# Performance work log

Hardware: AMD Instinct MI355X
Metric: run time of the kernel (lower is better)

Reference implementation:

```python
import jax, jax.numpy as jnp
import numpy as np

N = 8192
D = 2048      # input_dim
DH = 1024     # input_dim // r
DO = 1024     # output_dim

def setup_inputs() -> dict:
    key = jax.random.key(0)
    ks = jax.random.split(key, 11)
    s_in = 1.0 / np.sqrt(D)
    s_h = 1.0 / np.sqrt(DH)
    return {
        "O0": jax.random.normal(ks[0], (N, D), dtype=jnp.float32),
        "Ww": jax.random.uniform(ks[1], (DH, D), jnp.float32, -s_in, s_in),
        "Wb": jax.random.uniform(ks[2], (DH,), jnp.float32, -s_in, s_in),
        "Uw": jax.random.uniform(ks[3], (DH, D), jnp.float32, -s_in, s_in),
        "Ub": jax.random.uniform(ks[4], (DH,), jnp.float32, -s_in, s_in),
        "Hw": jax.random.uniform(ks[5], (DH, D), jnp.float32, -s_in, s_in),
        "Hb": jax.random.uniform(ks[6], (DH,), jnp.float32, -s_in, s_in),
        "fc0w": jax.random.uniform(ks[7], (D, DH), jnp.float32, -s_h, s_h),
        "fc0b": jax.random.uniform(ks[8], (D,), jnp.float32, -s_h, s_h),
        "fc1w": jax.random.uniform(ks[9], (DO, D), jnp.float32, -s_in, s_in),
        "fc1b": jax.random.uniform(ks[10], (DO,), jnp.float32, -s_in, s_in),
    }

def reference(O0, Ww, Wb, Uw, Ub, Hw, Hb, fc0w, fc0b, fc1w, fc1b):
    q = O0 @ Ww.T + Wb              # [N, DH]
    k = O0 @ Uw.T + Ub              # [N, DH]
    v = O0 @ Hw.T + Hb              # [N, DH]
    scores = q @ k.T                # [N, N], unscaled as in the original
    R1 = jax.nn.softmax(scores, axis=1)
    ctx = R1 @ v                    # [N, DH]
    O1 = O0 + (ctx @ fc0w.T + fc0b) # residual, [N, D]
    O2 = O1 @ fc1w.T + fc1b         # [N, DO]
    return (O1, O2)
```

## Files before the change

### kernel.cpp

```cpp
#include <hip/hip_runtime.h>
#include <cstdint>
#include <cstddef>

typedef _Float16 f16;
typedef _Float16 f16x8 __attribute__((ext_vector_type(8)));
typedef _Float16 f16x4 __attribute__((ext_vector_type(4)));
typedef float    f32x4 __attribute__((ext_vector_type(4)));

template <int V> struct IC { static constexpr int v = V; };

__global__ __launch_bounds__(256) void cvt_f32_f16(const float* __restrict__ in,
                                                   f16* __restrict__ out, int n) {
  int i = (blockIdx.x * 256 + threadIdx.x) * 4;
  if (i < n) {
    float4 v = *(const float4*)(in + i);
    f16x4 h; h[0] = (f16)v.x; h[1] = (f16)v.y; h[2] = (f16)v.z; h[3] = (f16)v.w;
    *(f16x4*)(out + i) = h;
  }
}

__global__ __launch_bounds__(256) void transpose_f16(const f16* __restrict__ in,
                                                     int ldi,
                                                     f16* __restrict__ out,
                                                     int R, int C) {
  __shared__ f16 tile[64][65];
  const int r0 = blockIdx.y * 64, c0 = blockIdx.x * 64;
  const int t = threadIdx.x;
#pragma unroll
  for (int p = 0; p < 2; p++) {
    int s = t + p * 256;
    int r = s >> 3, q = s & 7;
    f16x8 v = *(const f16x8*)(in + (size_t)(r0 + r) * ldi + c0 + q * 8);
#pragma unroll
    for (int e = 0; e < 8; e++) tile[r][q * 8 + e] = v[e];
  }
  __syncthreads();
#pragma unroll
  for (int p = 0; p < 2; p++) {
    int s = t + p * 256;
    int r = s >> 3, q = s & 7;
    f16x8 v;
#pragma unroll
    for (int e = 0; e < 8; e++) v[e] = tile[q * 8 + e][r];
    *(f16x8*)(out + (size_t)(c0 + r) * R + r0 + q * 8) = v;
  }
}

template <int MODE>
__global__ __launch_bounds__(512, 2) void gemm256(
    const f16* __restrict__ A, const f16* __restrict__ B,
    int M, int N, int K, int lda, int ldb,
    const float* __restrict__ bias,
    f16* __restrict__ outH, int ldo,
    float* __restrict__ statsM, float* __restrict__ statsS, int sld,
    const float* __restrict__ alphaT,
    const float* __restrict__ resid, int ldr,
    float* __restrict__ outF, int ldof) {
  __shared__ f16 lA[2][2][128 * 64];
  __shared__ f16 lB[2][2][128 * 64];
  __shared__ float lAl[2][256];

  const int t = threadIdx.x;
  const int wave = t >> 6, lane = t & 63;
  const int wr = wave >> 2, wc = wave & 3;
  const int quad = lane >> 4, l16 = lane & 15;
  const int rc = lane >> 3;
  const int kcs = (lane & 7) ^ rc;

  const int nwg = gridDim.x * gridDim.y;
  const int bid = blockIdx.y * gridDim.x + blockIdx.x;
  const int sb = (bid & 7) * (nwg >> 3) + (bid >> 3);
  const int bx = sb % gridDim.x, by = sb / gridDim.x;
  const int m0 = by * 256, n0 = bx * 256;
  const int nk = K >> 6;

  const f16* Abase = A + (size_t)m0 * lda;
  const f16* Bbase = B + (size_t)n0 * ldb;

  auto stageA = [&](int tau, int h) {
    if (tau >= nk) return;
    const f16* src = Abase + (size_t)(h * 128 + rc) * lda + tau * 64 + kcs * 8;
    f16* dstu = &lA[tau & 1][h][0];
#pragma unroll
    for (int j = 0; j < 2; j++) {
      const int sl = j * 8 + wave;
      __builtin_amdgcn_global_load_lds(
          (const __attribute__((address_space(1))) void*)(src + (size_t)sl * 8 * lda),
          (__attribute__((address_space(3))) void*)(dstu + sl * 512), 16, 0, 0);
    }
  };
  auto stageB = [&](int tau, int h) {
    if (tau >= nk) return;
    const f16* src = Bbase + (size_t)(h * 128 + rc) * ldb + tau * 64 + kcs * 8;
    f16* dstu = &lB[tau & 1][h][0];
#pragma unroll
    for (int j = 0; j < 2; j++) {
      const int sl = j * 8 + wave;
      __builtin_amdgcn_global_load_lds(
          (const __attribute__((address_space(1))) void*)(src + (size_t)sl * 8 * ldb),
          (__attribute__((address_space(3))) void*)(dstu + sl * 512), 16, 0, 0);
    }
  };
  auto stageAl = [&](int tau) {
    if constexpr (MODE == 2) {
      if (tau >= nk) return;
      __builtin_amdgcn_global_load_lds(
          (const __attribute__((address_space(1))) void*)(alphaT + (size_t)tau * M + m0 + lane * 4),
          (__attribute__((address_space(3))) void*)(&lAl[tau & 1][0]), 16, 0, 0);
    }
  };

  f32x4 acc[2][4][2][2];
#pragma unroll
  for (int mh = 0; mh < 2; mh++)
#pragma unroll
    for (int i = 0; i < 4; i++)
#pragma unroll
      for (int nh = 0; nh < 2; nh++)
#pragma unroll
        for (int j = 0; j < 2; j++)
#pragma unroll
          for (int e = 0; e < 4; e++) acc[mh][i][nh][j][e] = 0.0f;

  f16x8 af[4][2];
  f16x8 bf[2][2][2];

  auto readA = [&](auto BUFC, auto MHC) {
    constexpr int buf = decltype(BUFC)::v;
    constexpr int mh = decltype(MHC)::v;
#pragma unroll
    for (int i = 0; i < 4; i++) {
      const int r = i * 32 + wr * 16 + l16;
#pragma unroll
      for (int s = 0; s < 2; s++) {
        const int p = ((s * 4 + quad) ^ (l16 & 7)) * 8;
        af[i][s] = *(const f16x8*)(&lA[buf][mh][r * 64 + p]);
      }
      if constexpr (MODE == 2) {
        const f16 ah = (f16)lAl[buf][mh * 128 + r];
        af[i][0] = af[i][0] * ah;
        af[i][1] = af[i][1] * ah;
      }
    }
  };
  auto readB = [&](auto BUFC, auto NHC) {
    constexpr int buf = decltype(BUFC)::v;
    constexpr int nh = decltype(NHC)::v;
    const int hb = wc >> 1;
#pragma unroll
    for (int j = 0; j < 2; j++) {
      const int r = (wc & 1) * 64 + nh * 32 + j * 16 + l16;
#pragma unroll
      for (int s = 0; s < 2; s++) {
        const int p = ((s * 4 + quad) ^ (l16 & 7)) * 8;
        bf[nh][j][s] = *(const f16x8*)(&lB[buf][hb][r * 64 + p]);
      }
    }
  };
  auto mfmaQ = [&](auto MHC, auto NHC) {
    constexpr int mh = decltype(MHC)::v;
    constexpr int nh = decltype(NHC)::v;
    __builtin_amdgcn_s_setprio(1);
#pragma unroll
    for (int i = 0; i < 4; i++)
#pragma unroll
      for (int j = 0; j < 2; j++)
#pragma unroll
        for (int s = 0; s < 2; s++)
          acc[mh][i][nh][j] = __builtin_amdgcn_mfma_f32_16x16x32_f16(
              af[i][s], bf[nh][j][s], acc[mh][i][nh][j], 0, 0, 0);
    __builtin_amdgcn_s_setprio(0);
  };

  auto tile4 = [&](auto BUFC, int tt, bool dr) {
    readA(BUFC, IC<0>{});
    readB(BUFC, IC<0>{});
    stageA(tt + 1, 1);
    stageAl(tt + 1);
    __builtin_amdgcn_s_barrier();
    asm volatile("s_waitcnt lgkmcnt(0)" ::: "memory");
    mfmaQ(IC<0>{}, IC<0>{});
    __builtin_amdgcn_s_barrier();
    readB(BUFC, IC<1>{});
    stageA(tt + 2, 0);
    __builtin_amdgcn_s_barrier();
    asm volatile("s_waitcnt lgkmcnt(0)" ::: "memory");
    mfmaQ(IC<0>{}, IC<1>{});
    __builtin_amdgcn_s_barrier();
    readA(BUFC, IC<1>{});
    stageB(tt + 2, 0);
    __builtin_amdgcn_s_barrier();
    asm volatile("s_waitcnt lgkmcnt(0)" ::: "memory");
    mfmaQ(IC<1>{}, IC<1>{});
    __builtin_amdgcn_s_barrier();
    stageB(tt + 2, 1);
    __builtin_amdgcn_s_barrier();
    mfmaQ(IC<1>{}, IC<0>{});
    if (dr) { asm volatile("s_waitcnt vmcnt(0)" ::: "memory"); }
    else    { asm volatile("s_waitcnt vmcnt(6)" ::: "memory"); }
    __builtin_amdgcn_s_barrier();
  };

  stageA(0, 0); stageB(0, 0); stageB(0, 1); stageA(0, 1);
  stageAl(0);
  stageA(1, 0); stageB(1, 0); stageB(1, 1);
  asm volatile("s_waitcnt vmcnt(6)" ::: "memory");
  __builtin_amdgcn_s_barrier();

  for (int tt = 0; tt < nk; tt += 2) {
    const bool dr = (tt + 2 >= nk);
    tile4(IC<0>{}, tt, dr);
    tile4(IC<1>{}, tt + 1, dr);
  }

  const int colb = n0 + wc * 64 + l16;
  float bv[4];
  if constexpr (MODE == 0 || MODE == 3 || MODE == 4) {
#pragma unroll
    for (int c = 0; c < 4; c++) bv[c] = bias[colb + c * 16];
  }
#pragma unroll
  for (int mh = 0; mh < 2; mh++) {
#pragma unroll
    for (int i = 0; i < 4; i++) {
#pragma unroll
      for (int e = 0; e < 4; e++) {
        const int gr = m0 + mh * 128 + i * 32 + wr * 16 + quad * 4 + e;
        const float v0 = acc[mh][i][0][0][e];
        const float v1 = acc[mh][i][0][1][e];
        const float v2 = acc[mh][i][1][0][e];
        const float v3 = acc[mh][i][1][1][e];
        if constexpr (MODE == 1) {
          float mx = fmaxf(fmaxf(v0, v1), fmaxf(v2, v3));
          mx = fmaxf(mx, __shfl_xor(mx, 1));
          mx = fmaxf(mx, __shfl_xor(mx, 2));
          mx = fmaxf(mx, __shfl_xor(mx, 4));
          mx = fmaxf(mx, __shfl_xor(mx, 8));
          float e0 = __expf(v0 - mx);
          float e1 = __expf(v1 - mx);
          float e2 = __expf(v2 - mx);
          float e3 = __expf(v3 - mx);
          float sm = (e0 + e1) + (e2 + e3);
          sm += __shfl_xor(sm, 1);
          sm += __shfl_xor(sm, 2);
          sm += __shfl_xor(sm, 4);
          sm += __shfl_xor(sm, 8);
          if (l16 == 0) {
            statsM[(size_t)gr * sld + (bx * 4 + wc)] = mx;
            statsS[(size_t)gr * sld + (bx * 4 + wc)] = sm;
          }
          f16* rp = outH + (size_t)gr * ldo + colb;
          rp[0]  = (f16)e0;
          rp[16] = (f16)e1;
          rp[32] = (f16)e2;
          rp[48] = (f16)e3;
        } else if constexpr (MODE == 0) {
          f16* rp = outH + (size_t)gr * ldo + colb;
          rp[0]  = (f16)(v0 + bv[0]);
          rp[16] = (f16)(v1 + bv[1]);
          rp[32] = (f16)(v2 + bv[2]);
          rp[48] = (f16)(v3 + bv[3]);
        } else if constexpr (MODE == 2) {
          f16* rp = outH + (size_t)gr * ldo + colb;
          rp[0]  = (f16)v0;
          rp[16] = (f16)v1;
          rp[32] = (f16)v2;
          rp[48] = (f16)v3;
        } else if constexpr (MODE == 3) {
          float* rf = outF + (size_t)gr * ldof + colb;
          const float* rr = resid + (size_t)gr * ldr + colb;
          f16* rh = outH + (size_t)gr * ldo + colb;
          float o0 = v0 + bv[0] + rr[0];
          float o1 = v1 + bv[1] + rr[16];
          float o2 = v2 + bv[2] + rr[32];
          float o3 = v3 + bv[3] + rr[48];
          rf[0] = o0; rf[16] = o1; rf[32] = o2; rf[48] = o3;
          rh[0] = (f16)o0; rh[16] = (f16)o1; rh[32] = (f16)o2; rh[48] = (f16)o3;
        } else {
          float* rf = outF + (size_t)gr * ldof + colb;
          rf[0]  = v0 + bv[0];
          rf[16] = v1 + bv[1];
          rf[32] = v2 + bv[2];
          rf[48] = v3 + bv[3];
        }
      }
    }
  }
}

__global__ __launch_bounds__(256) void alpha_from_stats(
    const float* __restrict__ sM, const float* __restrict__ sS,
    float* __restrict__ aT, int rows) {
  __shared__ float alph[128][65];
  const int t = threadIdx.x;
  const int r = t >> 2, j = t & 3;
  const int row = blockIdx.x * 64 + r;
  const float* pm = sM + (size_t)row * 128 + j * 32;
  const float* ps = sS + (size_t)row * 128 + j * 32;
  float mv[32];
  float mx = -1e30f;
#pragma unroll
  for (int c = 0; c < 32; c++) { mv[c] = pm[c]; mx = fmaxf(mx, mv[c]); }
  mx = fmaxf(mx, __shfl_xor(mx, 1));
  mx = fmaxf(mx, __shfl_xor(mx, 2));
  float ev[32];
  float sum = 0.0f;
#pragma unroll
  for (int c = 0; c < 32; c++) {
    ev[c] = __expf(mv[c] - mx);
    sum += ev[c] * ps[c];
  }
  sum += __shfl_xor(sum, 1);
  sum += __shfl_xor(sum, 2);
  const float rl = 1.0f / sum;
#pragma unroll
  for (int c = 0; c < 32; c++) alph[j * 32 + c][r] = ev[c] * rl;
  __syncthreads();
  const int wid = t >> 6, rr = t & 63;
#pragma unroll
  for (int c = 0; c < 32; c++) {
    const int tg = c * 4 + wid;
    aT[(size_t)tg * rows + blockIdx.x * 64 + rr] = alph[tg][rr];
  }
}

extern "C" void kernel_launch(void* const* d_in, const int* in_sizes, int n_in,
                              void* d_out, int out_size, void* d_ws, size_t ws_size,
                              hipStream_t stream) {
  const float* O0   = (const float*)d_in[0];
  const float* Ww   = (const float*)d_in[1];
  const float* Wb   = (const float*)d_in[2];
  const float* Uw   = (const float*)d_in[3];
  const float* Ub   = (const float*)d_in[4];
  const float* Hw   = (const float*)d_in[5];
  const float* Hb   = (const float*)d_in[6];
  const float* fc0w = (const float*)d_in[7];
  const float* fc0b = (const float*)d_in[8];
  const float* fc1w = (const float*)d_in[9];
  const float* fc1b = (const float*)d_in[10];

  const int N = 8192, D = 2048, DH = 1024, DO = 1024;
  const int NQKV = 3 * DH;

  char* w = (char*)d_ws;
  f16* Wwh   = (f16*)w; w += (size_t)DH * D * 2;
  f16* Uwh   = (f16*)w; w += (size_t)DH * D * 2;
  f16* Hwh   = (f16*)w; w += (size_t)DH * D * 2;
  f16* fc0wh = (f16*)w; w += (size_t)D * DH * 2;
  f16* fc1wh = (f16*)w; w += (size_t)DO * D * 2;
  float* aT  = (float*)w; w += (size_t)128 * N * 4;
  char* un = w; w += (size_t)N * DH * 2;
  float* statsM = (float*)un;
  float* statsS = statsM + (size_t)N * 128;
  f16* ctxh = (f16*)un;
  float* biasC = (float*)w; w += (size_t)NQKV * 4;
  w = (char*)(((uintptr_t)w + 255) & ~(uintptr_t)255);
  f16* Sb = (f16*)w;

  f16* oh   = (f16*)d_out;
  f16* qkv  = oh;
  f16* qh   = qkv;
  f16* kh   = qkv + DH;
  f16* vh   = qkv + 2 * DH;
  f16* O0h  = oh + (size_t)N * NQKV;
  f16* vT   = O0h + (size_t)N * D;
  f16* O1h  = Sb;

  {
    int n = DH * D;
    int grid = n / 1024;
    cvt_f32_f16<<<grid, 256, 0, stream>>>(Ww, Wwh, n);
    cvt_f32_f16<<<grid, 256, 0, stream>>>(Uw, Uwh, n);
    cvt_f32_f16<<<grid, 256, 0, stream>>>(Hw, Hwh, n);
    cvt_f32_f16<<<grid, 256, 0, stream>>>(fc0w, fc0wh, n);
    cvt_f32_f16<<<grid, 256, 0, stream>>>(fc1w, fc1wh, n);
    cvt_f32_f16<<<(N * D) / 1024, 256, 0, stream>>>(O0, O0h, N * D);
    hipMemcpyAsync(biasC,          Wb, DH * 4, hipMemcpyDeviceToDevice, stream);
    hipMemcpyAsync(biasC + DH,     Ub, DH * 4, hipMemcpyDeviceToDevice, stream);
    hipMemcpyAsync(biasC + 2 * DH, Hb, DH * 4, hipMemcpyDeviceToDevice, stream);
  }

  gemm256<0><<<dim3(NQKV / 256, N / 256), 512, 0, stream>>>(
      O0h, Wwh, N, NQKV, D, D, D, biasC,
      qkv, NQKV, nullptr, nullptr, 0, nullptr, nullptr, 0, nullptr, 0);

  transpose_f16<<<dim3(DH / 64, N / 64), 256, 0, stream>>>(vh, NQKV, vT, N, DH);

  gemm256<1><<<dim3(N / 256, N / 256), 512, 0, stream>>>(
      qh, kh, N, N, DH, NQKV, NQKV, nullptr, Sb, N,
      statsM, statsS, 128, nullptr, nullptr, 0, nullptr, 0);

  alpha_from_stats<<<N / 64, 256, 0, stream>>>(statsM, statsS, aT, N);

  gemm256<2><<<dim3(DH / 256, N / 256), 512, 0, stream>>>(
      Sb, vT, N, DH, N, N, N, nullptr, ctxh, DH,
      nullptr, nullptr, 0, aT, nullptr, 0, nullptr, 0);

  gemm256<3><<<dim3(D / 256, N / 256), 512, 0, stream>>>(
      ctxh, fc0wh, N, D, DH, DH, DH, fc0b, O1h, D,
      nullptr, nullptr, 0, nullptr, O0, D, (float*)d_out, D);

  gemm256<4><<<dim3(DO / 256, N / 256), 512, 0, stream>>>(
      O1h, fc1wh, N, DO, D, D, D, fc1b, nullptr, 0,
      nullptr, nullptr, 0, nullptr, nullptr, 0,
      (float*)d_out + (size_t)N * D, DO);
}
```

Baseline: 874.8 us.

## Add 256x128-tile GEMM kernel for narrow-N PV and fc1 products

Introduces a gemmN128 kernel with 256x128 output tiles, double-buffered direct-to-LDS loads and fused alpha scaling (PV) or bias (fc1) epilogues. It is used for the context GEMM and the final fc1 GEMM, whose 1024-wide outputs produced only 128 workgroups with 256x256 tiles. Doubling the workgroup count is meant to fill all compute units. The trade-off is less operand reuse per tile and more A-matrix traffic.

```diff
diff --git a/kernel.cpp b/kernel.cpp
--- a/kernel.cpp
+++ b/kernel.cpp
@@ -288,6 +288,186 @@
   }
 }
 
+template <int MODE>
+__global__ __launch_bounds__(512, 2) void gemmN128(
+    const f16* __restrict__ A, const f16* __restrict__ B,
+    int M, int N, int K, int lda, int ldb,
+    const float* __restrict__ bias,
+    f16* __restrict__ outH, int ldo,
+    const float* __restrict__ alphaT,
+    float* __restrict__ outF, int ldof) {
+  __shared__ f16 lA[2][2][128 * 64];
+  __shared__ f16 lB[2][128 * 64];
+  __shared__ float lAl[2][256];
+
+  const int t = threadIdx.x;
+  const int wave = t >> 6, lane = t & 63;
+  const int wr = wave >> 1, wc = wave & 1;
+  const int quad = lane >> 4, l16 = lane & 15;
+  const int rc = lane >> 3;
+  const int kcs = (lane & 7) ^ rc;
+
+  const int nwg = gridDim.x * gridDim.y;
+  const int bid = blockIdx.y * gridDim.x + blockIdx.x;
+  const int sb = (bid & 7) * (nwg >> 3) + (bid >> 3);
+  const int bx = sb % gridDim.x, by = sb / gridDim.x;
+  const int m0 = by * 256, n0 = bx * 128;
+  const int nk = K >> 6;
+
+  const f16* Abase = A + (size_t)m0 * lda;
+  const f16* Bbase = B + (size_t)n0 * ldb;
+
+  auto stageA = [&](int tau, int h) {
+    if (tau >= nk) return;
+    const f16* src = Abase + (size_t)(h * 128 + rc) * lda + tau * 64 + kcs * 8;
+    f16* dstu = &lA[tau & 1][h][0];
+#pragma unroll
+    for (int j = 0; j < 2; j++) {
+      const int sl = j * 8 + wave;
+      __builtin_amdgcn_global_load_lds(
+          (const __attribute__((address_space(1))) void*)(src + (size_t)sl * 8 * lda),
+          (__attribute__((address_space(3))) void*)(dstu + sl * 512), 16, 0, 0);
+    }
+  };
+  auto stageB = [&](int tau) {
+    if (tau >= nk) return;
+    const f16* src = Bbase + (size_t)rc * ldb + tau * 64 + kcs * 8;
+    f16* dstu = &lB[tau & 1][0];
+#pragma unroll
+    for (int j = 0; j < 2; j++) {
+      const int sl = j * 8 + wave;
+      __builtin_amdgcn_global_load_lds(
+          (const __attribute__((address_space(1))) void*)(src + (size_t)sl * 8 * ldb),
+          (__attribute__((address_space(3))) void*)(dstu + sl * 512), 16, 0, 0);
+    }
+  };
+  auto stageAl = [&](int tau) {
+    if constexpr (MODE == 2) {
+      if (tau >= nk) return;
+      __builtin_amdgcn_global_load_lds(
+          (const __attribute__((address_space(1))) void*)(alphaT + (size_t)tau * M + m0 + lane * 4),
+          (__attribute__((address_space(3))) void*)(&lAl[tau & 1][0]), 16, 0, 0);
+    }
+  };
+
+  f32x4 acc[4][2][2];
+#pragma unroll
+  for (int i = 0; i < 4; i++)
+#pragma unroll
+    for (int nh = 0; nh < 2; nh++)
+#pragma unroll
+      for (int j = 0; j < 2; j++)
+#pragma unroll
+        for (int e = 0; e < 4; e++) acc[i][nh][j][e] = 0.0f;
+
+  f16x8 af[4][2];
+  f16x8 bf[2][2][2];
+  const int ha = wr >> 1;
+
+  auto readA = [&](auto BUFC) {
+    constexpr int buf = decltype(BUFC)::v;
+#pragma unroll
+    for (int i = 0; i < 4; i++) {
+      const int r = (wr & 1) * 64 + i * 16 + l16;
+#pragma unroll
+      for (int s = 0; s < 2; s++) {
+        const int p = ((s * 4 + quad) ^ (l16 & 7)) * 8;
+        af[i][s] = *(const f16x8*)(&lA[buf][ha][r * 64 + p]);
+      }
+      if constexpr (MODE == 2) {
+        const f16 ah = (f16)lAl[buf][wr * 64 + i * 16 + l16];
+        af[i][0] = af[i][0] * ah;
+        af[i][1] = af[i][1] * ah;
+      }
+    }
+  };
+  auto readB = [&](auto BUFC, auto NHC) {
+    constexpr int buf = decltype(BUFC)::v;
+    constexpr int nh = decltype(NHC)::v;
+#pragma unroll
+    for (int j = 0; j < 2; j++) {
+      const int r = wc * 64 + nh * 32 + j * 16 + l16;
+#pragma unroll
+      for (int s = 0; s < 2; s++) {
+        const int p = ((s * 4 + quad) ^ (l16 & 7)) * 8;
+        bf[nh][j][s] = *(const f16x8*)(&lB[buf][r * 64 + p]);
+      }
+    }
+  };
+  auto mfmaQ = [&](auto NHC) {
+    constexpr int nh = decltype(NHC)::v;
+    __builtin_amdgcn_s_setprio(1);
+#pragma unroll
+    for (int i = 0; i < 4; i++)
+#pragma unroll
+      for (int j = 0; j < 2; j++)
+#pragma unroll
+        for (int s = 0; s < 2; s++)
+          acc[i][nh][j] = __builtin_amdgcn_mfma_f32_16x16x32_f16(
+              af[i][s], bf[nh][j][s], acc[i][nh][j], 0, 0, 0);
+    __builtin_amdgcn_s_setprio(0);
+  };
+
+  auto tile2 = [&](auto BUFC, int tt, bool dr) {
+    readA(BUFC);
+    readB(BUFC, IC<0>{});
+    readB(BUFC, IC<1>{});
+    stageA(tt + 1, 1);
+    stageAl(tt + 1);
+    __builtin_amdgcn_s_barrier();
+    asm volatile("s_waitcnt lgkmcnt(0)" ::: "memory");
+    mfmaQ(IC<0>{});
+    __builtin_amdgcn_s_barrier();
+    stageA(tt + 2, 0);
+    stageB(tt + 2);
+    __builtin_amdgcn_s_barrier();
+    mfmaQ(IC<1>{});
+    if (dr) { asm volatile("s_waitcnt vmcnt(0)" ::: "memory"); }
+    else    { asm volatile("s_waitcnt vmcnt(4)" ::: "memory"); }
+    __builtin_amdgcn_s_barrier();
+  };
+
+  stageA(0, 0); stageB(0); stageA(0, 1); stageAl(0);
+  stageA(1, 0); stageB(1);
+  asm volatile("s_waitcnt vmcnt(4)" ::: "memory");
+  __builtin_amdgcn_s_barrier();
+
+  for (int tt = 0; tt < nk; tt += 2) {
+    const bool dr = (tt + 2 >= nk);
+    tile2(IC<0>{}, tt, dr);
+    tile2(IC<1>{}, tt + 1, dr);
+  }
+
+  float bv[2][2];
+  if constexpr (MODE == 4) {
+#pragma unroll
+    for (int nh = 0; nh < 2; nh++)
+#pragma unroll
+      for (int j = 0; j < 2; j++)
+        bv[nh][j] = bias[n0 + wc * 64 + nh * 32 + j * 16 + l16];
+  }
+#pragma unroll
+  for (int i = 0; i < 4; i++) {
+#pragma unroll
+    for (int e = 0; e < 4; e++) {
+      const int gr = m0 + wr * 64 + i * 16 + quad * 4 + e;
+#pragma unroll
+      for (int nh = 0; nh < 2; nh++) {
+#pragma unroll
+        for (int j = 0; j < 2; j++) {
+          const int col = n0 + wc * 64 + nh * 32 + j * 16 + l16;
+          const float v = acc[i][nh][j][e];
+          if constexpr (MODE == 2) {
+            outH[(size_t)gr * ldo + col] = (f16)v;
+          } else {
+            outF[(size_t)gr * ldof + col] = v + bv[nh][j];
+          }
+        }
+      }
+    }
+  }
+}
+
 __global__ __launch_bounds__(256) void alpha_from_stats(
     const float* __restrict__ sM, const float* __restrict__ sS,
     float* __restrict__ aT, int rows) {
@@ -392,16 +572,14 @@
 
   alpha_from_stats<<<N / 64, 256, 0, stream>>>(statsM, statsS, aT, N);
 
-  gemm256<2><<<dim3(DH / 256, N / 256), 512, 0, stream>>>(
-      Sb, vT, N, DH, N, N, N, nullptr, ctxh, DH,
-      nullptr, nullptr, 0, aT, nullptr, 0, nullptr, 0);
+  gemmN128<2><<<dim3(DH / 128, N / 256), 512, 0, stream>>>(
+      Sb, vT, N, DH, N, N, N, nullptr, ctxh, DH, aT, nullptr, 0);
 
   gemm256<3><<<dim3(D / 256, N / 256), 512, 0, stream>>>(
       ctxh, fc0wh, N, D, DH, DH, DH, fc0b, O1h, D,
       nullptr, nullptr, 0, nullptr, O0, D, (float*)d_out, D);
 
-  gemm256<4><<<dim3(DO / 256, N / 256), 512, 0, stream>>>(
-      O1h, fc1wh, N, DO, D, D, D, fc1b, nullptr, 0,
-      nullptr, nullptr, 0, nullptr, nullptr, 0,
+  gemmN128<4><<<dim3(DO / 128, N / 256), 512, 0, stream>>>(
+      O1h, fc1wh, N, DO, D, D, D, fc1b, nullptr, 0, nullptr,
       (float*)d_out + (size_t)N * D, DO);
 }
```

After: 759.4 us. 1.15x faster.
